# Kernel tuning notes

Hardware: AMD Instinct MI355X
Metric: run time of the kernel (lower is better)

Reference implementation:

```python
import jax, jax.numpy as jnp
import numpy as np

N = 100000          # nodes
E = 1600000         # edges (nnz of A)
D_IN = 128
D_OUT = 128


def setup_inputs() -> dict:
    key = jax.random.key(0)
    ks = jax.random.split(key, 9)
    s = 1.0 / np.sqrt(D_IN)
    inp = {
        "h_n": jax.random.normal(ks[0], (N, D_IN), dtype=jnp.float32),
        "W_w": jax.random.uniform(ks[1], (D_OUT, D_IN), jnp.float32, -s, s),
        "W_b": jax.random.uniform(ks[2], (D_OUT,), jnp.float32, -s, s),
        "Wt_w": jax.random.uniform(ks[3], (D_OUT, D_IN), jnp.float32, -s, s),
        "Wt_b": jax.random.uniform(ks[4], (D_OUT,), jnp.float32, -s, s),
        "Ws_w": jax.random.uniform(ks[5], (D_OUT, D_IN), jnp.float32, -s, s),
        "Ws_b": jax.random.uniform(ks[6], (D_OUT,), jnp.float32, -s, s),
        # COO indices of sparse adjacency A (binary values): A[rows[e], cols[e]] = 1
        "rows": jax.random.randint(ks[7], (E,), 0, N, dtype=jnp.int64)
                if jax.config.jax_enable_x64 else
                jax.random.randint(ks[7], (E,), 0, N, dtype=jnp.int32),
        "cols": jax.random.randint(ks[8], (E,), 0, N, dtype=jnp.int32),
    }
    inp["rows"] = inp["rows"].astype(jnp.int32)
    return inp


def reference(h_n, W_w, W_b, Wt_w, Wt_b, Ws_w, Ws_b, rows, cols):
    # Dense projections: [N, D_OUT]
    Wh  = h_n @ W_w.T + W_b    # W(h_n)
    Wth = h_n @ Wt_w.T + Wt_b  # W_trans(h_n)
    Wsh = h_n @ Ws_w.T + Ws_b  # W_self(h_n)

    # A @ Wh  : out[i] = sum over edges (i=rows[e], j=cols[e]) of Wh[j]
    agg   = jax.ops.segment_sum(Wh[cols],  rows, num_segments=N)
    # A_T @ Wth : out[i] = sum over edges (j=rows[e], i=cols[e]) of Wth[j]
    agg_t = jax.ops.segment_sum(Wth[rows], cols, num_segments=N)

    # exact (erf-based) GELU, matching torch F.gelu default
    return jax.nn.gelu(agg + agg_t + Wsh, approximate=False)
```

## Files before the change

kernel.cpp:

```cpp
#include <hip/hip_runtime.h>


typedef __bf16 bf16;
typedef __bf16 bf16x4 __attribute__((ext_vector_type(4)));
typedef __bf16 bf16x8 __attribute__((ext_vector_type(8)));
typedef float  f32x4  __attribute__((ext_vector_type(4)));
typedef unsigned int u32;
typedef u32 u32x2 __attribute__((ext_vector_type(2)));

#define D 128
#define CAPC 2432
#define SLAB 2560
#define BIN_CHUNK 12544

__global__ void k_cast(const float* __restrict__ src, bf16* __restrict__ dst, int n4) {
    int i = blockIdx.x * 256 + threadIdx.x;
    if (i < n4) {
        f32x4 v = *(const f32x4*)&src[i * 4];
        bf16x4 o;
        o.x = (bf16)v.x; o.y = (bf16)v.y; o.z = (bf16)v.z; o.w = (bf16)v.w;
        *(bf16x4*)&dst[i * 4] = o;
    }
}

__global__ __launch_bounds__(256) void k_bin(
    const int* __restrict__ rows, const int* __restrict__ cols,
    int* __restrict__ gcnt_f, int* __restrict__ gcnt_r,
    u32* __restrict__ buf_f, u32* __restrict__ buf_r, int E, int B) {
    __shared__ int hist[1024];
    __shared__ int lbase[1024];
    __shared__ int gbase[1024];
    __shared__ int tsum[256];
    __shared__ u32 sorted[BIN_CHUNK];
    int t = threadIdx.x;
    int dir = blockIdx.y;
    const int* key = dir ? cols : rows;
    const int* pay = dir ? rows : cols;
    int* gcnt = dir ? gcnt_r : gcnt_f;
    u32* buf  = dir ? buf_r : buf_f;
    int base = blockIdx.x * BIN_CHUNK;

    for (int b = t; b < 1024; b += 256) hist[b] = 0;
    __syncthreads();
    for (int i = 0; i < BIN_CHUNK / 256; ++i) {
        int e = base + i * 256 + t;
        if (e < E) atomicAdd(&hist[key[e] >> 7], 1);
    }
    __syncthreads();
    int s0 = hist[t * 4], s1 = hist[t * 4 + 1], s2 = hist[t * 4 + 2], s3 = hist[t * 4 + 3];
    tsum[t] = s0 + s1 + s2 + s3;
    __syncthreads();
    for (int o = 1; o < 256; o <<= 1) {
        int v = (t >= o) ? tsum[t - o] : 0;
        __syncthreads();
        tsum[t] += v;
        __syncthreads();
    }
    int run = (t > 0) ? tsum[t - 1] : 0;
    lbase[t * 4]     = run;
    lbase[t * 4 + 1] = run + s0;
    lbase[t * 4 + 2] = run + s0 + s1;
    lbase[t * 4 + 3] = run + s0 + s1 + s2;
    __syncthreads();
    int total = tsum[255];
    for (int b = t; b < 1024; b += 256) {
        int nxt = (b < 1023) ? lbase[b + 1] : total;
        int c = nxt - lbase[b];
        gbase[b] = (c && b < B) ? atomicAdd(&gcnt[b], c) : 0;
        hist[b] = lbase[b];
    }
    __syncthreads();
    for (int i = 0; i < BIN_CHUNK / 256; ++i) {
        int e = base + i * 256 + t;
        if (e < E) {
            int k = key[e], p = pay[e];
            int pos = atomicAdd(&hist[k >> 7], 1);
            sorted[pos] = ((u32)(k & 127) << 17) | (u32)p;
        }
    }
    __syncthreads();
    for (int b = t; b < B; b += 256) {
        int lb = lbase[b];
        int nxt = (b < 1023) ? lbase[b + 1] : total;
        int c = nxt - lb;
        if (!c) continue;
        int gb = gbase[b];
        u32* dst = buf + (size_t)b * SLAB;
        for (int i = 0; i < c; ++i) {
            int gp = gb + i;
            if (gp < CAPC) dst[gp] = sorted[lb + i];
        }
    }
}

__global__ __launch_bounds__(256) void k_sort(
    const int* __restrict__ cnt_f, const int* __restrict__ cnt_r,
    u32* __restrict__ buf_f, u32* __restrict__ buf_r,
    int* __restrict__ off_f, int* __restrict__ off_r,
    int* __restrict__ deg_f, int* __restrict__ deg_r, int N, u32 PADV) {
    __shared__ u32 words[CAPC];
    __shared__ u32 sorted[SLAB];
    __shared__ int hist[128], pscn[128], cur[128];
    int t = threadIdx.x, bkt = blockIdx.x;
    const int* cp; u32* buf; int* off; int* deg;
    if (blockIdx.y == 0) { cp = cnt_f; buf = buf_f + (size_t)bkt * SLAB; off = off_f; deg = deg_f; }
    else                 { cp = cnt_r; buf = buf_r + (size_t)bkt * SLAB; off = off_r; deg = deg_r; }
    int cnt = cp[bkt]; if (cnt > CAPC) cnt = CAPC;
    if (t < 128) hist[t] = 0;
    __syncthreads();
    for (int i = t; i < cnt; i += 256) {
        u32 w = buf[i]; words[i] = w;
        atomicAdd(&hist[w >> 17], 1);
    }
    __syncthreads();
    int pd = 0;
    if (t < 128) { pd = (hist[t] + 1) & ~1; pscn[t] = pd; }
    __syncthreads();
    for (int o = 1; o < 128; o <<= 1) {
        int v = (t < 128 && t >= o) ? pscn[t - o] : 0;
        __syncthreads();
        if (t < 128) pscn[t] += v;
        __syncthreads();
    }
    int ptot = pscn[127];
    int node0 = bkt * 128;
    if (t < 128) {
        int pstart = pscn[t] - pd;
        cur[t] = pstart;
        int node = node0 + t;
        if (node < N) { off[node] = bkt * SLAB + pstart; deg[node] = hist[t]; }
    }
    __syncthreads();
    for (int i = t; i < ptot; i += 256) sorted[i] = PADV;
    __syncthreads();
    for (int i = t; i < cnt; i += 256) {
        u32 w = words[i];
        int p = atomicAdd(&cur[w >> 17], 1);
        sorted[p] = w & 0x1FFFF;
    }
    __syncthreads();
    for (int i = t; i < ptot; i += 256) buf[i] = sorted[i];
}

__device__ __forceinline__ float blo(u32 w) { return __uint_as_float(w << 16); }
__device__ __forceinline__ float bhi(u32 w) { return __uint_as_float(w & 0xffff0000u); }

__global__ void k_agg(const bf16* __restrict__ h,
                      const int* __restrict__ off_f, const int* __restrict__ deg_f,
                      const u32* __restrict__ buf_f,
                      const int* __restrict__ off_r, const int* __restrict__ deg_r,
                      const u32* __restrict__ buf_r,
                      bf16* __restrict__ AH, bf16* __restrict__ ATH, int N) {
    int wave = threadIdx.x >> 6, lane = threadIdx.x & 63;
    int node = blockIdx.x * 4 + wave;
    if (node >= N) return;
    const int* off; const int* deg; const u32* idx; bf16* dst;
    if (blockIdx.y == 0) { off = off_f; deg = deg_f; idx = buf_f; dst = AH; }
    else                 { off = off_r; deg = deg_r; idx = buf_r; dst = ATH; }
    int p = off[node];
    int pend = p + ((deg[node] + 1) & ~1);
    int half = lane >> 5, col = lane & 31;
    const u32* h32 = (const u32*)h;
    float a0 = 0.f, a1 = 0.f, a2 = 0.f, a3 = 0.f;
    for (; p + 7 < pend; p += 8) {
        u32 j[4];
#pragma unroll
        for (int u = 0; u < 4; ++u) j[u] = idx[p + 2 * u + half];
#pragma unroll
        for (int u = 0; u < 4; ++u) {
            u32x2 w = *(const u32x2*)&h32[(size_t)j[u] * 64 + col * 2];
            a0 += blo(w.x); a1 += bhi(w.x);
            a2 += blo(w.y); a3 += bhi(w.y);
        }
    }
    for (; p + 1 < pend; p += 2) {
        u32 j = idx[p + half];
        u32x2 w = *(const u32x2*)&h32[(size_t)j * 64 + col * 2];
        a0 += blo(w.x); a1 += bhi(w.x);
        a2 += blo(w.y); a3 += bhi(w.y);
    }
    a0 += __shfl_down(a0, 32);
    a1 += __shfl_down(a1, 32);
    a2 += __shfl_down(a2, 32);
    a3 += __shfl_down(a3, 32);
    if (half == 0) {
        bf16x4 o;
        o.x = (bf16)a0; o.y = (bf16)a1; o.z = (bf16)a2; o.w = (bf16)a3;
        *(bf16x4*)&dst[(size_t)node * D + col * 4] = o;
    }
}

__global__ __launch_bounds__(256) void k_gemm(
    const bf16* __restrict__ h, const bf16* __restrict__ AH, const bf16* __restrict__ ATH,
    const float* __restrict__ Ws_w, const float* __restrict__ W_w, const float* __restrict__ Wt_w,
    const float* __restrict__ Ws_b, const float* __restrict__ W_b, const float* __restrict__ Wt_b,
    const int* __restrict__ deg_out, const int* __restrict__ deg_in,
    float* __restrict__ out, int N) {
    __shared__ __align__(16) bf16 Ash[128 * 32];
    __shared__ __align__(16) bf16 Bsh[128 * 32];
    int t = threadIdx.x;
    int lane = t & 63;
    int w = t >> 6;
    int wm = (w >> 1) * 64, wn = (w & 1) * 64;
    int m0 = blockIdx.x * 128;

    f32x4 acc[4][4];
#pragma unroll
    for (int i = 0; i < 4; ++i)
#pragma unroll
        for (int j = 0; j < 4; ++j)
            acc[i][j] = (f32x4){0.f, 0.f, 0.f, 0.f};

    for (int kc = 0; kc < 12; ++kc) {
        const bf16*  X  = (kc < 4) ? h    : (kc < 8) ? AH  : ATH;
        const float* Wm = (kc < 4) ? Ws_w : (kc < 8) ? W_w : Wt_w;
        int c0 = (kc & 3) * 32;
#pragma unroll
        for (int r = 0; r < 2; ++r) {
            int v = r * 256 + t;
            int row = v >> 2, seg = v & 3;
            int xr = m0 + row; if (xr >= N) xr = N - 1;
            *(bf16x8*)&Ash[row * 32 + seg * 8] =
                *(const bf16x8*)&X[(size_t)xr * D + c0 + seg * 8];
        }
#pragma unroll
        for (int r = 0; r < 4; ++r) {
            int v = r * 256 + t;
            int row = v >> 3, seg = v & 7;
            f32x4 f = *(const f32x4*)&Wm[row * D + c0 + seg * 4];
            bf16x4 o;
            o.x = (bf16)f.x; o.y = (bf16)f.y; o.z = (bf16)f.z; o.w = (bf16)f.w;
            *(bf16x4*)&Bsh[row * 32 + seg * 4] = o;
        }
        __syncthreads();
        int kg = lane >> 4, lr = lane & 15;
        bf16x8 a[4], b[4];
#pragma unroll
        for (int i = 0; i < 4; ++i) {
            a[i] = *(const bf16x8*)&Ash[(wm + i * 16 + lr) * 32 + kg * 8];
            b[i] = *(const bf16x8*)&Bsh[(wn + i * 16 + lr) * 32 + kg * 8];
        }
#pragma unroll
        for (int i = 0; i < 4; ++i)
#pragma unroll
            for (int j = 0; j < 4; ++j)
                acc[i][j] = __builtin_amdgcn_mfma_f32_16x16x32_bf16(
                    a[i], b[j], acc[i][j], 0, 0, 0);
        __syncthreads();
    }

    int lr = lane & 15, lq = lane >> 4;
#pragma unroll
    for (int i = 0; i < 4; ++i) {
#pragma unroll
        for (int r = 0; r < 4; ++r) {
            int node = m0 + wm + i * 16 + lq * 4 + r;
            if (node >= N) continue;
            float fdr = (float)deg_out[node], fdc = (float)deg_in[node];
#pragma unroll
            for (int j = 0; j < 4; ++j) {
                int f = wn + j * 16 + lr;
                float val = acc[i][j][r] + Ws_b[f] + fdr * W_b[f] + fdc * Wt_b[f];
                float g = 0.5f * val * (1.0f + erff(val * 0.70710678118654752f));
                out[(size_t)node * D + f] = g;
            }
        }
    }
}

extern "C" void kernel_launch(void* const* d_in, const int* in_sizes, int n_in,
                              void* d_out, int out_size, void* d_ws, size_t ws_size,
                              hipStream_t stream) {
    const float* h    = (const float*)d_in[0];
    const float* W_w  = (const float*)d_in[1];
    const float* W_b  = (const float*)d_in[2];
    const float* Wt_w = (const float*)d_in[3];
    const float* Wt_b = (const float*)d_in[4];
    const float* Ws_w = (const float*)d_in[5];
    const float* Ws_b = (const float*)d_in[6];
    const int*   rows = (const int*)d_in[7];
    const int*   cols = (const int*)d_in[8];
    float* out = (float*)d_out;

    const int N = in_sizes[0] / D;
    const int E = in_sizes[7];
    const int B = (N + 127) >> 7;

    char* ws = (char*)d_ws;
    size_t off = 0;
    auto take = [&](size_t bytes) -> char* {
        char* p = ws + off;
        off += (bytes + 511) & ~(size_t)511;
        return p;
    };
    bf16* h_bf    = (bf16*)take((size_t)(N + 1) * D * sizeof(bf16));
    bf16* AH      = (bf16*)take((size_t)N * D * sizeof(bf16));
    bf16* ATH     = (bf16*)take((size_t)N * D * sizeof(bf16));
    int*  gcnt    = (int*)take((size_t)2 * B * sizeof(int));
    int*  off_f   = (int*)take((size_t)N * sizeof(int));
    int*  off_r   = (int*)take((size_t)N * sizeof(int));
    int*  deg_f   = (int*)take((size_t)N * sizeof(int));
    int*  deg_r   = (int*)take((size_t)N * sizeof(int));
    u32*  buf_f   = (u32*)take((size_t)B * SLAB * sizeof(u32));
    u32*  buf_r   = (u32*)take((size_t)B * SLAB * sizeof(u32));
    int*  gcnt_f = gcnt, *gcnt_r = gcnt + B;

    hipMemsetAsync(gcnt, 0, (size_t)2 * B * sizeof(int), stream);
    hipMemsetAsync(h_bf + (size_t)N * D, 0, D * sizeof(bf16), stream);

    int n4 = N * D / 4;
    k_cast<<<(n4 + 255) / 256, 256, 0, stream>>>(h, h_bf, n4);

    dim3 gbin((E + BIN_CHUNK - 1) / BIN_CHUNK, 2);
    k_bin<<<gbin, 256, 0, stream>>>(rows, cols, gcnt_f, gcnt_r, buf_f, buf_r, E, B);
    dim3 gsort(B, 2);
    k_sort<<<gsort, 256, 0, stream>>>(gcnt_f, gcnt_r, buf_f, buf_r,
                                      off_f, off_r, deg_f, deg_r, N, (u32)N);
    dim3 gagg((N + 3) / 4, 2);
    k_agg<<<gagg, 256, 0, stream>>>(h_bf, off_f, deg_f, buf_f,
                                    off_r, deg_r, buf_r, AH, ATH, N);
    k_gemm<<<B, 256, 0, stream>>>(h_bf, AH, ATH,
                                  Ws_w, W_w, Wt_w,
                                  Ws_b, W_b, Wt_b,
                                  deg_f, deg_r, out, N);
}
```

Baseline: 347.8 us.

## Widen aggregation gathers, parallelize bin scatter, precast weights to bf16

The aggregation kernel now splits each wave into four quarter-wave groups that gather 16-byte rows per lane. Per-node edge lists are padded to multiples of four, and indices are pre-shifted into row word offsets. The binning kernel's per-bucket serial copy-out is replaced by a fully parallel scatter that uses per-element bucket tags in shared memory. The three weight matrices are cast to bf16 once in the cast kernel rather than in every GEMM tile, which also removes a memset. The cost is larger padding slabs and extra shared memory in the bin kernel, which may reduce occupancy.

```diff
diff --git a/kernel.cpp b/kernel.cpp
--- a/kernel.cpp
+++ b/kernel.cpp
@@ -6,20 +6,38 @@
 typedef __bf16 bf16x8 __attribute__((ext_vector_type(8)));
 typedef float  f32x4  __attribute__((ext_vector_type(4)));
 typedef unsigned int u32;
-typedef u32 u32x2 __attribute__((ext_vector_type(2)));
+typedef u32 u32x4 __attribute__((ext_vector_type(4)));
+typedef unsigned short u16;
 
 #define D 128
 #define CAPC 2432
-#define SLAB 2560
+#define SLAB 2816
 #define BIN_CHUNK 12544
 
-__global__ void k_cast(const float* __restrict__ src, bf16* __restrict__ dst, int n4) {
+__global__ void k_cast(const float* __restrict__ h,
+                       const float* __restrict__ Ws_w, const float* __restrict__ W_w,
+                       const float* __restrict__ Wt_w,
+                       bf16* __restrict__ h_bf, bf16* __restrict__ wbf, int n4h) {
     int i = blockIdx.x * 256 + threadIdx.x;
-    if (i < n4) {
-        f32x4 v = *(const f32x4*)&src[i * 4];
+    if (i < n4h) {
+        f32x4 v = *(const f32x4*)&h[i * 4];
         bf16x4 o;
         o.x = (bf16)v.x; o.y = (bf16)v.y; o.z = (bf16)v.z; o.w = (bf16)v.w;
-        *(bf16x4*)&dst[i * 4] = o;
+        *(bf16x4*)&h_bf[i * 4] = o;
+    } else if (i < n4h + 32) {
+        int k = i - n4h;
+        bf16x4 z; z.x = (bf16)0.f; z.y = (bf16)0.f; z.z = (bf16)0.f; z.w = (bf16)0.f;
+        *(bf16x4*)&h_bf[(size_t)n4h * 4 + k * 4] = z;
+    } else {
+        int k = i - n4h - 32;
+        if (k < 12288) {
+            const float* src = (k < 4096) ? Ws_w : (k < 8192) ? W_w : Wt_w;
+            int kk = k & 4095;
+            f32x4 v = *(const f32x4*)&src[kk * 4];
+            bf16x4 o;
+            o.x = (bf16)v.x; o.y = (bf16)v.y; o.z = (bf16)v.z; o.w = (bf16)v.w;
+            *(bf16x4*)&wbf[k * 4] = o;
+        }
     }
 }
 
@@ -32,6 +50,7 @@
     __shared__ int gbase[1024];
     __shared__ int tsum[256];
     __shared__ u32 sorted[BIN_CHUNK];
+    __shared__ u16 btag[BIN_CHUNK];
     int t = threadIdx.x;
     int dir = blockIdx.y;
     const int* key = dir ? cols : rows;
@@ -74,22 +93,17 @@
         int e = base + i * 256 + t;
         if (e < E) {
             int k = key[e], p = pay[e];
-            int pos = atomicAdd(&hist[k >> 7], 1);
+            int b = k >> 7;
+            int pos = atomicAdd(&hist[b], 1);
             sorted[pos] = ((u32)(k & 127) << 17) | (u32)p;
-        }
-    }
-    __syncthreads();
-    for (int b = t; b < B; b += 256) {
-        int lb = lbase[b];
-        int nxt = (b < 1023) ? lbase[b + 1] : total;
-        int c = nxt - lb;
-        if (!c) continue;
-        int gb = gbase[b];
-        u32* dst = buf + (size_t)b * SLAB;
-        for (int i = 0; i < c; ++i) {
-            int gp = gb + i;
-            if (gp < CAPC) dst[gp] = sorted[lb + i];
-        }
+            btag[pos] = (u16)b;
+        }
+    }
+    __syncthreads();
+    for (int i = t; i < total; i += 256) {
+        int b = btag[i];
+        int gp = gbase[b] + (i - lbase[b]);
+        if (gp < CAPC) buf[(size_t)b * SLAB + gp] = sorted[i];
     }
 }
 
@@ -114,7 +128,7 @@
     }
     __syncthreads();
     int pd = 0;
-    if (t < 128) { pd = (hist[t] + 1) & ~1; pscn[t] = pd; }
+    if (t < 128) { pd = (hist[t] + 3) & ~3; pscn[t] = pd; }
     __syncthreads();
     for (int o = 1; o < 128; o <<= 1) {
         int v = (t < 128 && t >= o) ? pscn[t - o] : 0;
@@ -136,7 +150,7 @@
     for (int i = t; i < cnt; i += 256) {
         u32 w = words[i];
         int p = atomicAdd(&cur[w >> 17], 1);
-        sorted[p] = w & 0x1FFFF;
+        sorted[p] = (w & 0x1FFFF) << 6;
     }
     __syncthreads();
     for (int i = t; i < ptot; i += 256) buf[i] = sorted[i];
@@ -145,7 +159,7 @@
 __device__ __forceinline__ float blo(u32 w) { return __uint_as_float(w << 16); }
 __device__ __forceinline__ float bhi(u32 w) { return __uint_as_float(w & 0xffff0000u); }
 
-__global__ void k_agg(const bf16* __restrict__ h,
+__global__ void k_agg(const u32* __restrict__ h32,
                       const int* __restrict__ off_f, const int* __restrict__ deg_f,
                       const u32* __restrict__ buf_f,
                       const int* __restrict__ off_r, const int* __restrict__ deg_r,
@@ -158,41 +172,51 @@
     if (blockIdx.y == 0) { off = off_f; deg = deg_f; idx = buf_f; dst = AH; }
     else                 { off = off_r; deg = deg_r; idx = buf_r; dst = ATH; }
     int p = off[node];
-    int pend = p + ((deg[node] + 1) & ~1);
-    int half = lane >> 5, col = lane & 31;
-    const u32* h32 = (const u32*)h;
+    int pend = p + ((deg[node] + 3) & ~3);
+    int q = lane >> 4, c = lane & 15;
     float a0 = 0.f, a1 = 0.f, a2 = 0.f, a3 = 0.f;
-    for (; p + 7 < pend; p += 8) {
-        u32 j[4];
-#pragma unroll
-        for (int u = 0; u < 4; ++u) j[u] = idx[p + 2 * u + half];
-#pragma unroll
-        for (int u = 0; u < 4; ++u) {
-            u32x2 w = *(const u32x2*)&h32[(size_t)j[u] * 64 + col * 2];
-            a0 += blo(w.x); a1 += bhi(w.x);
-            a2 += blo(w.y); a3 += bhi(w.y);
-        }
-    }
-    for (; p + 1 < pend; p += 2) {
-        u32 j = idx[p + half];
-        u32x2 w = *(const u32x2*)&h32[(size_t)j * 64 + col * 2];
-        a0 += blo(w.x); a1 += bhi(w.x);
-        a2 += blo(w.y); a3 += bhi(w.y);
-    }
-    a0 += __shfl_down(a0, 32);
-    a1 += __shfl_down(a1, 32);
-    a2 += __shfl_down(a2, 32);
-    a3 += __shfl_down(a3, 32);
-    if (half == 0) {
-        bf16x4 o;
-        o.x = (bf16)a0; o.y = (bf16)a1; o.z = (bf16)a2; o.w = (bf16)a3;
-        *(bf16x4*)&dst[(size_t)node * D + col * 4] = o;
+    float a4 = 0.f, a5 = 0.f, a6 = 0.f, a7 = 0.f;
+    for (; p + 15 < pend; p += 16) {
+        u32 j0 = idx[p + q], j1 = idx[p + 4 + q];
+        u32 j2 = idx[p + 8 + q], j3 = idx[p + 12 + q];
+        u32x4 w0 = *(const u32x4*)&h32[(size_t)j0 + c * 4];
+        u32x4 w1 = *(const u32x4*)&h32[(size_t)j1 + c * 4];
+        u32x4 w2 = *(const u32x4*)&h32[(size_t)j2 + c * 4];
+        u32x4 w3 = *(const u32x4*)&h32[(size_t)j3 + c * 4];
+        a0 += blo(w0.x); a1 += bhi(w0.x); a2 += blo(w0.y); a3 += bhi(w0.y);
+        a4 += blo(w0.z); a5 += bhi(w0.z); a6 += blo(w0.w); a7 += bhi(w0.w);
+        a0 += blo(w1.x); a1 += bhi(w1.x); a2 += blo(w1.y); a3 += bhi(w1.y);
+        a4 += blo(w1.z); a5 += bhi(w1.z); a6 += blo(w1.w); a7 += bhi(w1.w);
+        a0 += blo(w2.x); a1 += bhi(w2.x); a2 += blo(w2.y); a3 += bhi(w2.y);
+        a4 += blo(w2.z); a5 += bhi(w2.z); a6 += blo(w2.w); a7 += bhi(w2.w);
+        a0 += blo(w3.x); a1 += bhi(w3.x); a2 += blo(w3.y); a3 += bhi(w3.y);
+        a4 += blo(w3.z); a5 += bhi(w3.z); a6 += blo(w3.w); a7 += bhi(w3.w);
+    }
+    for (; p + 3 < pend; p += 4) {
+        u32 j = idx[p + q];
+        u32x4 w = *(const u32x4*)&h32[(size_t)j + c * 4];
+        a0 += blo(w.x); a1 += bhi(w.x); a2 += blo(w.y); a3 += bhi(w.y);
+        a4 += blo(w.z); a5 += bhi(w.z); a6 += blo(w.w); a7 += bhi(w.w);
+    }
+    a0 += __shfl_down(a0, 16); a1 += __shfl_down(a1, 16);
+    a2 += __shfl_down(a2, 16); a3 += __shfl_down(a3, 16);
+    a4 += __shfl_down(a4, 16); a5 += __shfl_down(a5, 16);
+    a6 += __shfl_down(a6, 16); a7 += __shfl_down(a7, 16);
+    a0 += __shfl_down(a0, 32); a1 += __shfl_down(a1, 32);
+    a2 += __shfl_down(a2, 32); a3 += __shfl_down(a3, 32);
+    a4 += __shfl_down(a4, 32); a5 += __shfl_down(a5, 32);
+    a6 += __shfl_down(a6, 32); a7 += __shfl_down(a7, 32);
+    if (lane < 16) {
+        bf16x8 o;
+        o[0] = (bf16)a0; o[1] = (bf16)a1; o[2] = (bf16)a2; o[3] = (bf16)a3;
+        o[4] = (bf16)a4; o[5] = (bf16)a5; o[6] = (bf16)a6; o[7] = (bf16)a7;
+        *(bf16x8*)&dst[(size_t)node * D + c * 8] = o;
     }
 }
 
 __global__ __launch_bounds__(256) void k_gemm(
     const bf16* __restrict__ h, const bf16* __restrict__ AH, const bf16* __restrict__ ATH,
-    const float* __restrict__ Ws_w, const float* __restrict__ W_w, const float* __restrict__ Wt_w,
+    const bf16* __restrict__ wbf,
     const float* __restrict__ Ws_b, const float* __restrict__ W_b, const float* __restrict__ Wt_b,
     const int* __restrict__ deg_out, const int* __restrict__ deg_in,
     float* __restrict__ out, int N) {
@@ -212,8 +236,8 @@
             acc[i][j] = (f32x4){0.f, 0.f, 0.f, 0.f};
 
     for (int kc = 0; kc < 12; ++kc) {
-        const bf16*  X  = (kc < 4) ? h    : (kc < 8) ? AH  : ATH;
-        const float* Wm = (kc < 4) ? Ws_w : (kc < 8) ? W_w : Wt_w;
+        const bf16* X  = (kc < 4) ? h : (kc < 8) ? AH : ATH;
+        const bf16* Wm = wbf + (kc >> 2) * (128 * 128);
         int c0 = (kc & 3) * 32;
 #pragma unroll
         for (int r = 0; r < 2; ++r) {
@@ -222,15 +246,8 @@
             int xr = m0 + row; if (xr >= N) xr = N - 1;
             *(bf16x8*)&Ash[row * 32 + seg * 8] =
                 *(const bf16x8*)&X[(size_t)xr * D + c0 + seg * 8];
-        }
-#pragma unroll
-        for (int r = 0; r < 4; ++r) {
-            int v = r * 256 + t;
-            int row = v >> 3, seg = v & 7;
-            f32x4 f = *(const f32x4*)&Wm[row * D + c0 + seg * 4];
-            bf16x4 o;
-            o.x = (bf16)f.x; o.y = (bf16)f.y; o.z = (bf16)f.z; o.w = (bf16)f.w;
-            *(bf16x4*)&Bsh[row * 32 + seg * 4] = o;
+            *(bf16x8*)&Bsh[row * 32 + seg * 8] =
+                *(const bf16x8*)&Wm[row * D + c0 + seg * 8];
         }
         __syncthreads();
         int kg = lane >> 4, lr = lane & 15;
@@ -296,6 +313,7 @@
     bf16* h_bf    = (bf16*)take((size_t)(N + 1) * D * sizeof(bf16));
     bf16* AH      = (bf16*)take((size_t)N * D * sizeof(bf16));
     bf16* ATH     = (bf16*)take((size_t)N * D * sizeof(bf16));
+    bf16* wbf     = (bf16*)take((size_t)3 * 128 * 128 * sizeof(bf16));
     int*  gcnt    = (int*)take((size_t)2 * B * sizeof(int));
     int*  off_f   = (int*)take((size_t)N * sizeof(int));
     int*  off_r   = (int*)take((size_t)N * sizeof(int));
@@ -306,21 +324,21 @@
     int*  gcnt_f = gcnt, *gcnt_r = gcnt + B;
 
     hipMemsetAsync(gcnt, 0, (size_t)2 * B * sizeof(int), stream);
-    hipMemsetAsync(h_bf + (size_t)N * D, 0, D * sizeof(bf16), stream);
-
-    int n4 = N * D / 4;
-    k_cast<<<(n4 + 255) / 256, 256, 0, stream>>>(h, h_bf, n4);
+
+    int n4h = N * D / 4;
+    int ncast = n4h + 32 + 3 * 128 * 128 / 4;
+    k_cast<<<(ncast + 255) / 256, 256, 0, stream>>>(h, Ws_w, W_w, Wt_w,
+                                                    h_bf, wbf, n4h);
 
     dim3 gbin((E + BIN_CHUNK - 1) / BIN_CHUNK, 2);
     k_bin<<<gbin, 256, 0, stream>>>(rows, cols, gcnt_f, gcnt_r, buf_f, buf_r, E, B);
     dim3 gsort(B, 2);
     k_sort<<<gsort, 256, 0, stream>>>(gcnt_f, gcnt_r, buf_f, buf_r,
-                                      off_f, off_r, deg_f, deg_r, N, (u32)N);
+                                      off_f, off_r, deg_f, deg_r, N, (u32)N << 6);
     dim3 gagg((N + 3) / 4, 2);
-    k_agg<<<gagg, 256, 0, stream>>>(h_bf, off_f, deg_f, buf_f,
+    k_agg<<<gagg, 256, 0, stream>>>((const u32*)h_bf, off_f, deg_f, buf_f,
                                     off_r, deg_r, buf_r, AH, ATH, N);
-    k_gemm<<<B, 256, 0, stream>>>(h_bf, AH, ATH,
-                                  Ws_w, W_w, Wt_w,
+    k_gemm<<<B, 256, 0, stream>>>(h_bf, AH, ATH, wbf,
                                   Ws_b, W_b, Wt_b,
                                   deg_f, deg_r, out, N);
 }
```

After: 329.7 us. 5.2% less time.
